# Optimization experiments

Hardware: AMD Instinct MI355X
Metric: run time of the kernel (lower is better)

Reference implementation:

```python
import jax, jax.numpy as jnp
import numpy as np

N_NODES = 100000
N_EDGES = 1600000
IN_CH = 64
OUT_CH = 64
NUM_K = 9  # (degree+1)^dim = 3*3 quadratic B-spline taps; equals prod(kernel_size) here


def _quad_basis(v):
    # torch_spline_conv quadratic basis for k_mod in {0,1,2}; v = frac(pseudo*(K-deg)) = pseudo here
    return jnp.stack([0.5 * v * v - v + 0.5,
                      -v * v + v + 0.5,
                      0.5 * v * v], axis=-1)  # [E,3]


def spline_conv(x, src, dst, pseudo, W, root, bias, n_nodes):
    # W: [9, C_in, C_out]; basis B: [E, 9]
    b0 = _quad_basis(pseudo[:, 0])          # [E,3]
    b1 = _quad_basis(pseudo[:, 1])          # [E,3]
    B = (b0[:, :, None] * b1[:, None, :]).reshape(pseudo.shape[0], NUM_K)  # [E,9]
    x_src = x[src]                           # gather [E, C_in]
    msg = B[:, 0:1] * (x_src @ W[0])
    for k in range(1, NUM_K):                # fixed small loop over kernel taps
        msg = msg + B[:, k:k + 1] * (x_src @ W[k])
    out = jax.ops.segment_sum(msg, dst, num_segments=n_nodes)  # scatter-add at targets
    return out + x @ root + bias


def setup_inputs() -> dict:
    key = jax.random.key(0)
    ks = jax.random.split(key, 10)
    x = jax.random.normal(ks[0], (N_NODES, IN_CH), dtype=jnp.float32)
    edge_index = jax.random.randint(ks[1], (2, N_EDGES), 0, N_NODES, dtype=jnp.int64)
    pseudo = jax.random.uniform(ks[2], (N_EDGES, 2), dtype=jnp.float32)
    s1 = 1.0 / np.sqrt(IN_CH * NUM_K)
    s2 = 1.0 / np.sqrt(OUT_CH * NUM_K)
    W1 = jax.random.normal(ks[3], (NUM_K, IN_CH, OUT_CH), dtype=jnp.float32) * s1
    root1 = jax.random.normal(ks[4], (IN_CH, OUT_CH), dtype=jnp.float32) * s1
    b1 = jax.random.normal(ks[5], (OUT_CH,), dtype=jnp.float32) * 0.01
    W2 = jax.random.normal(ks[6], (NUM_K, OUT_CH, OUT_CH), dtype=jnp.float32) * s2
    root2 = jax.random.normal(ks[7], (OUT_CH, OUT_CH), dtype=jnp.float32) * s2
    b2 = jax.random.normal(ks[8], (OUT_CH,), dtype=jnp.float32) * 0.01
    return {"x": x, "edge_index": edge_index, "pseudo": pseudo,
            "W1": W1, "root1": root1, "b1": b1,
            "W2": W2, "root2": root2, "b2": b2}


def reference(x, edge_index, pseudo, W1, root1, b1, W2, root2, b2):
    src, dst = edge_index[0], edge_index[1]  # PyG: aggregate messages at target
    h = jax.nn.relu(spline_conv(x, src, dst, pseudo, W1, root1, b1, N_NODES))
    h = jax.nn.relu(spline_conv(h, src, dst, pseudo, W2, root2, b2, N_NODES))
    return h
```

## Files before the change

### kernel.cpp

```cpp
#include <hip/hip_runtime.h>
#include <stdint.h>

typedef __attribute__((ext_vector_type(8))) short bf16x8;
typedef __attribute__((ext_vector_type(4))) float f32x4;

__device__ __forceinline__ float bf2f(unsigned short u) {
  union { unsigned int i; float f; } x; x.i = ((unsigned int)u) << 16; return x.f;
}
__device__ __forceinline__ unsigned short f2bf(float f) {
  union { float f; unsigned int i; } x; x.f = f;
  unsigned int i = x.i;
  return (unsigned short)((i + 0x7FFFu + ((i >> 16) & 1u)) >> 16);
}


__global__ void count_kernel(const int* __restrict__ ei, int E, int* __restrict__ counts) {
  int e = blockIdx.x * blockDim.x + threadIdx.x;
  if (e < E) atomicAdd(&counts[ei[E + e]], 1);
}

__global__ void scan1_kernel(const int* __restrict__ counts, int n, int* __restrict__ bsum) {
  int i = blockIdx.x * 256 + threadIdx.x;
  int v = (i < n) ? counts[i] : 0;
  int lane = threadIdx.x & 63, w = threadIdx.x >> 6;
  for (int d = 32; d > 0; d >>= 1) v += __shfl_down(v, d, 64);
  __shared__ int ws[4];
  if (lane == 0) ws[w] = v;
  __syncthreads();
  if (threadIdx.x == 0) bsum[blockIdx.x] = ws[0] + ws[1] + ws[2] + ws[3];
}

__global__ void scan2_kernel(int* __restrict__ bsum, int G) {
  int t = threadIdx.x;
  int c = (G + 511) >> 9;
  int lo = min(t * c, G), hi = min(lo + c, G);
  int s = 0;
  for (int i = lo; i < hi; ++i) s += bsum[i];
  int lane = t & 63, w = t >> 6;
  int incl = s;
  for (int d = 1; d < 64; d <<= 1) { int u = __shfl_up(incl, d, 64); if (lane >= d) incl += u; }
  __shared__ int wsum[8];
  if (lane == 63) wsum[w] = incl;
  __syncthreads();
  int wpre = 0;
  for (int i = 0; i < w; ++i) wpre += wsum[i];
  int excl = wpre + incl - s;
  for (int i = lo; i < hi; ++i) { int v = bsum[i]; bsum[i] = excl; excl += v; }
}

__global__ void scan3_kernel(const int* __restrict__ counts, int n, const int* __restrict__ bsum,
                             int* __restrict__ offsets, int* __restrict__ cursor, int total) {
  int i = blockIdx.x * 256 + threadIdx.x;
  int v = (i < n) ? counts[i] : 0;
  int lane = threadIdx.x & 63, w = threadIdx.x >> 6;
  int incl = v;
  for (int d = 1; d < 64; d <<= 1) { int u = __shfl_up(incl, d, 64); if (lane >= d) incl += u; }
  __shared__ int wsum[4];
  if (lane == 63) wsum[w] = incl;
  __syncthreads();
  int pre = bsum[blockIdx.x];
  for (int j = 0; j < w; ++j) pre += wsum[j];
  if (i < n) {
    int excl = pre + incl - v;
    offsets[i] = excl;
    cursor[i] = excl;
  }
  if (i == 0) offsets[n] = total;
}


__global__ void fill_kernel(const int* __restrict__ ei, const float* __restrict__ pseudo,
                            int E, int* __restrict__ cursor, int* __restrict__ src_s,
                            float2* __restrict__ bas) {
  int e = blockIdx.x * blockDim.x + threadIdx.x;
  if (e >= E) return;
  int d = ei[E + e];
  int s = ei[e];
  float2 uv = ((const float2*)pseudo)[e];
  float u = uv.x, v = uv.y;
  float b0 = 0.5f * u * u - u + 0.5f, b1 = -u * u + u + 0.5f, b2 = 0.5f * u * u;
  float c0 = 0.5f * v * v - v + 0.5f, c1 = -v * v + v + 0.5f, c2 = 0.5f * v * v;
  int p = atomicAdd(&cursor[d], 1);
  src_s[p] = s;
  size_t o = (size_t)p * 3;
  bas[o + 0] = make_float2(b0, b1);
  bas[o + 1] = make_float2(b2, c0);
  bas[o + 2] = make_float2(c1, c2);
}


__global__ void wconv_kernel(const float* __restrict__ W, const float* __restrict__ root,
                             unsigned short* __restrict__ Wt) {
  int i = blockIdx.x * blockDim.x + threadIdx.x;
  if (i >= 640 * 64) return;
  int co = i / 640, r = i % 640;
  float v = (r < 576) ? W[r * 64 + co] : root[(r - 576) * 64 + co];
  Wt[i] = f2bf(v);
}


__global__ void xconv_kernel(const float4* __restrict__ x4, ushort4* __restrict__ xh4, int n4) {
  int i = blockIdx.x * blockDim.x + threadIdx.x;
  if (i < n4) {
    float4 v = x4[i];
    ushort4 o;
    o.x = f2bf(v.x); o.y = f2bf(v.y); o.z = f2bf(v.z); o.w = f2bf(v.w);
    xh4[i] = o;
  }
}


#define SROW 648

#define EDGE_FMA(Q0, Q1, Q2, XV)                                   \
  {                                                                \
    float t0 = Q0.x * XV, t1 = Q0.y * XV, t2 = Q1.x * XV;          \
    a0 += t0 * Q1.y; a1 += t0 * Q2.x; a2 += t0 * Q2.y;             \
    a3 += t1 * Q1.y; a4 += t1 * Q2.x; a5 += t1 * Q2.y;             \
    a6 += t2 * Q1.y; a7 += t2 * Q2.x; a8 += t2 * Q2.y;             \
  }

template <bool OUTBF16>
__global__ __launch_bounds__(256) void fused_kernel(const int* __restrict__ offsets,
                                                    const int* __restrict__ src_s,
                                                    const float2* __restrict__ bas,
                                                    const unsigned short* __restrict__ Xh,
                                                    const unsigned short* __restrict__ Wt,
                                                    const float* __restrict__ bias,
                                                    void* __restrict__ outv, int N) {
  __shared__ short sA[16 * SROW];
  int tid = threadIdx.x, w = tid >> 6, lane = tid & 63;
  int nodeBase = blockIdx.x * 16;

  for (int t = 0; t < 4; ++t) {
    int row = w * 4 + t;
    int n = nodeBase + row;
    if (n >= N) continue;
    int beg = __builtin_amdgcn_readfirstlane(offsets[n]);
    int end = __builtin_amdgcn_readfirstlane(offsets[n + 1]);
    float a0 = 0.f, a1 = 0.f, a2 = 0.f, a3 = 0.f, a4 = 0.f,
          a5 = 0.f, a6 = 0.f, a7 = 0.f, a8 = 0.f;
    int j = beg;
    for (; j + 4 <= end; j += 4) {
      int s0 = src_s[j], s1 = src_s[j + 1], s2 = src_s[j + 2], s3 = src_s[j + 3];
      size_t o = (size_t)j * 3;
      float2 q00 = bas[o + 0], q01 = bas[o + 1], q02 = bas[o + 2];
      float2 q10 = bas[o + 3], q11 = bas[o + 4], q12 = bas[o + 5];
      float2 q20 = bas[o + 6], q21 = bas[o + 7], q22 = bas[o + 8];
      float2 q30 = bas[o + 9], q31 = bas[o + 10], q32 = bas[o + 11];
      float xv0 = bf2f(Xh[(size_t)s0 * 64 + lane]);
      float xv1 = bf2f(Xh[(size_t)s1 * 64 + lane]);
      float xv2 = bf2f(Xh[(size_t)s2 * 64 + lane]);
      float xv3 = bf2f(Xh[(size_t)s3 * 64 + lane]);
      EDGE_FMA(q00, q01, q02, xv0);
      EDGE_FMA(q10, q11, q12, xv1);
      EDGE_FMA(q20, q21, q22, xv2);
      EDGE_FMA(q30, q31, q32, xv3);
    }
    for (; j < end; ++j) {
      int s0 = src_s[j];
      size_t o = (size_t)j * 3;
      float2 q00 = bas[o + 0], q01 = bas[o + 1], q02 = bas[o + 2];
      float xv0 = bf2f(Xh[(size_t)s0 * 64 + lane]);
      EDGE_FMA(q00, q01, q02, xv0);
    }
    float self = bf2f(Xh[(size_t)n * 64 + lane]);
    int rb = row * SROW;
    sA[rb + 0 * 64 + lane] = (short)f2bf(a0);
    sA[rb + 1 * 64 + lane] = (short)f2bf(a1);
    sA[rb + 2 * 64 + lane] = (short)f2bf(a2);
    sA[rb + 3 * 64 + lane] = (short)f2bf(a3);
    sA[rb + 4 * 64 + lane] = (short)f2bf(a4);
    sA[rb + 5 * 64 + lane] = (short)f2bf(a5);
    sA[rb + 6 * 64 + lane] = (short)f2bf(a6);
    sA[rb + 7 * 64 + lane] = (short)f2bf(a7);
    sA[rb + 8 * 64 + lane] = (short)f2bf(a8);
    sA[rb + 576 + lane] = (short)f2bf(self);
  }
  __syncthreads();

  int r15 = lane & 15, kg = lane >> 4;
  f32x4 acc = {0.f, 0.f, 0.f, 0.f};
#pragma unroll
  for (int kk = 0; kk < 20; ++kk) {
    int kbase = kk * 32 + kg * 8;
    bf16x8 af = *(const bf16x8*)(&sA[r15 * SROW + kbase]);
    bf16x8 bfr = *(const bf16x8*)(Wt + (size_t)(w * 16 + r15) * 640 + kbase);
    acc = __builtin_amdgcn_mfma_f32_16x16x32_bf16(af, bfr, acc, 0, 0, 0);
  }
  int col = w * 16 + r15;
  float bv = bias[col];
  int row0 = kg * 4;
#pragma unroll
  for (int r = 0; r < 4; ++r) {
    int node = nodeBase + row0 + r;
    if (node < N) {
      float val = fmaxf(acc[r] + bv, 0.f);
      size_t idx = (size_t)node * 64 + col;
      if (OUTBF16) ((unsigned short*)outv)[idx] = f2bf(val);
      else ((float*)outv)[idx] = val;
    }
  }
}


extern "C" void kernel_launch(void* const* d_in, const int* in_sizes, int n_in,
                              void* d_out, int out_size, void* d_ws, size_t ws_size,
                              hipStream_t stream) {
  const float* x = (const float*)d_in[0];
  const int* ei = (const int*)d_in[1];
  const float* pseudo = (const float*)d_in[2];
  const float* W1 = (const float*)d_in[3];
  const float* root1 = (const float*)d_in[4];
  const float* b1 = (const float*)d_in[5];
  const float* W2 = (const float*)d_in[6];
  const float* root2 = (const float*)d_in[7];
  const float* b2 = (const float*)d_in[8];

  const int N = in_sizes[0] / 64;
  const int E = in_sizes[1] / 2;
  const int G = (N + 255) / 256;

  char* p = (char*)d_ws;
  auto carve = [&](size_t bytes) -> void* {
    void* r = (void*)p;
    p += (bytes + 255) & ~(size_t)255;
    return r;
  };
  int* counts = (int*)carve((size_t)N * 4);
  int* offsets = (int*)carve((size_t)(N + 1) * 4);
  int* cursor = (int*)carve((size_t)N * 4);
  int* bsum = (int*)carve((size_t)G * 4);
  int* src_s = (int*)carve((size_t)E * 4);
  float2* bas = (float2*)carve((size_t)E * 24);
  unsigned short* Wt1 = (unsigned short*)carve(640 * 64 * 2);
  unsigned short* Wt2 = (unsigned short*)carve(640 * 64 * 2);
  unsigned short* h = (unsigned short*)carve((size_t)N * 64 * 2);
  unsigned short* xh = (unsigned short*)carve((size_t)N * 64 * 2);
  (void)ws_size;

  hipMemsetAsync(counts, 0, (size_t)N * 4, stream);
  count_kernel<<<(E + 255) / 256, 256, 0, stream>>>(ei, E, counts);
  scan1_kernel<<<G, 256, 0, stream>>>(counts, N, bsum);
  scan2_kernel<<<1, 512, 0, stream>>>(bsum, G);
  scan3_kernel<<<G, 256, 0, stream>>>(counts, N, bsum, offsets, cursor, E);
  fill_kernel<<<(E + 255) / 256, 256, 0, stream>>>(ei, pseudo, E, cursor, src_s, bas);
  wconv_kernel<<<160, 256, 0, stream>>>(W1, root1, Wt1);
  wconv_kernel<<<160, 256, 0, stream>>>(W2, root2, Wt2);
  xconv_kernel<<<(N * 16 + 255) / 256, 256, 0, stream>>>((const float4*)x, (ushort4*)xh, N * 16);

  int FB = (N + 15) / 16;
  fused_kernel<true><<<FB, 256, 0, stream>>>(offsets, src_s, bas, xh, Wt1, b1, (void*)h, N);
  fused_kernel<false><<<FB, 256, 0, stream>>>(offsets, src_s, bas, h, Wt2, b2, d_out, N);
}
```

Measured before the change: 428.6 us.

## Pack edge records into 16-byte fp16 structs and double-buffer 8-edge loads

Replaces the separate src index array and 24-byte float basis array with one 16-byte record per edge: a pre-shifted byte offset plus six fp16 basis factors. Each record then comes from a single vector load. The gather loop now prefetches 8 records ahead with double buffering to overlap latency. Blocks grow to 512 threads, so each wave handles 2 nodes instead of 4, and only 4 of the 8 waves run the MFMA stage. The change cuts edge-stream bytes and raises memory parallelism, at the cost of fp16 precision on the basis values and idle waves during the matmul.

```diff
diff --git a/kernel.cpp b/kernel.cpp
--- a/kernel.cpp
+++ b/kernel.cpp
@@ -11,6 +11,19 @@
   union { float f; unsigned int i; } x; x.f = f;
   unsigned int i = x.i;
   return (unsigned short)((i + 0x7FFFu + ((i >> 16) & 1u)) >> 16);
+}
+__device__ __forceinline__ float f16lo(unsigned int u) {
+  union { unsigned short s; _Float16 h; } x; x.s = (unsigned short)(u & 0xFFFFu);
+  return (float)x.h;
+}
+__device__ __forceinline__ float f16hi(unsigned int u) {
+  union { unsigned short s; _Float16 h; } x; x.s = (unsigned short)(u >> 16);
+  return (float)x.h;
+}
+__device__ __forceinline__ unsigned int packf16(float a, float b) {
+  union { unsigned short s; _Float16 h; } x, y;
+  x.h = (_Float16)a; y.h = (_Float16)b;
+  return (unsigned int)x.s | ((unsigned int)y.s << 16);
 }
 
 
@@ -70,8 +83,7 @@
 
 
 __global__ void fill_kernel(const int* __restrict__ ei, const float* __restrict__ pseudo,
-                            int E, int* __restrict__ cursor, int* __restrict__ src_s,
-                            float2* __restrict__ bas) {
+                            int E, int* __restrict__ cursor, uint4* __restrict__ recs) {
   int e = blockIdx.x * blockDim.x + threadIdx.x;
   if (e >= E) return;
   int d = ei[E + e];
@@ -81,11 +93,12 @@
   float b0 = 0.5f * u * u - u + 0.5f, b1 = -u * u + u + 0.5f, b2 = 0.5f * u * u;
   float c0 = 0.5f * v * v - v + 0.5f, c1 = -v * v + v + 0.5f, c2 = 0.5f * v * v;
   int p = atomicAdd(&cursor[d], 1);
-  src_s[p] = s;
-  size_t o = (size_t)p * 3;
-  bas[o + 0] = make_float2(b0, b1);
-  bas[o + 1] = make_float2(b2, c0);
-  bas[o + 2] = make_float2(c1, c2);
+  uint4 r;
+  r.x = ((unsigned int)s) << 7;
+  r.y = packf16(b0, b1);
+  r.z = packf16(b2, c0);
+  r.w = packf16(c1, c2);
+  recs[p] = r;
 }
 
 
@@ -112,18 +125,27 @@
 
 #define SROW 648
 
-#define EDGE_FMA(Q0, Q1, Q2, XV)                                   \
-  {                                                                \
-    float t0 = Q0.x * XV, t1 = Q0.y * XV, t2 = Q1.x * XV;          \
-    a0 += t0 * Q1.y; a1 += t0 * Q2.x; a2 += t0 * Q2.y;             \
-    a3 += t1 * Q1.y; a4 += t1 * Q2.x; a5 += t1 * Q2.y;             \
-    a6 += t2 * Q1.y; a7 += t2 * Q2.x; a8 += t2 * Q2.y;             \
+#define LOAD8(R, jj)                                                     \
+  _Pragma("unroll") for (int k = 0; k < 8; ++k) R[k] = recs[(size_t)(jj) + k];
+
+#define PROC8(R)                                                         \
+  {                                                                      \
+    float xv[8];                                                         \
+    _Pragma("unroll") for (int k = 0; k < 8; ++k)                        \
+        xv[k] = bf2f(*(const unsigned short*)(Xb + R[k].x + laneB));     \
+    _Pragma("unroll") for (int k = 0; k < 8; ++k) {                      \
+      float b0 = f16lo(R[k].y), b1 = f16hi(R[k].y), b2 = f16lo(R[k].z);  \
+      float c0 = f16hi(R[k].z), c1 = f16lo(R[k].w), c2 = f16hi(R[k].w);  \
+      float t0 = b0 * xv[k], t1 = b1 * xv[k], t2 = b2 * xv[k];           \
+      a0 += t0 * c0; a1 += t0 * c1; a2 += t0 * c2;                       \
+      a3 += t1 * c0; a4 += t1 * c1; a5 += t1 * c2;                       \
+      a6 += t2 * c0; a7 += t2 * c1; a8 += t2 * c2;                       \
+    }                                                                    \
   }
 
 template <bool OUTBF16>
-__global__ __launch_bounds__(256) void fused_kernel(const int* __restrict__ offsets,
-                                                    const int* __restrict__ src_s,
-                                                    const float2* __restrict__ bas,
+__global__ __launch_bounds__(512) void fused_kernel(const int* __restrict__ offsets,
+                                                    const uint4* __restrict__ recs,
                                                     const unsigned short* __restrict__ Xh,
                                                     const unsigned short* __restrict__ Wt,
                                                     const float* __restrict__ bias,
@@ -131,74 +153,80 @@
   __shared__ short sA[16 * SROW];
   int tid = threadIdx.x, w = tid >> 6, lane = tid & 63;
   int nodeBase = blockIdx.x * 16;
-
-  for (int t = 0; t < 4; ++t) {
-    int row = w * 4 + t;
+  const char* Xb = (const char*)Xh;
+  unsigned int laneB = (unsigned int)lane * 2u;
+
+#pragma unroll
+  for (int t = 0; t < 2; ++t) {
+    int row = w * 2 + t;
     int n = nodeBase + row;
-    if (n >= N) continue;
-    int beg = __builtin_amdgcn_readfirstlane(offsets[n]);
-    int end = __builtin_amdgcn_readfirstlane(offsets[n + 1]);
-    float a0 = 0.f, a1 = 0.f, a2 = 0.f, a3 = 0.f, a4 = 0.f,
-          a5 = 0.f, a6 = 0.f, a7 = 0.f, a8 = 0.f;
-    int j = beg;
-    for (; j + 4 <= end; j += 4) {
-      int s0 = src_s[j], s1 = src_s[j + 1], s2 = src_s[j + 2], s3 = src_s[j + 3];
-      size_t o = (size_t)j * 3;
-      float2 q00 = bas[o + 0], q01 = bas[o + 1], q02 = bas[o + 2];
-      float2 q10 = bas[o + 3], q11 = bas[o + 4], q12 = bas[o + 5];
-      float2 q20 = bas[o + 6], q21 = bas[o + 7], q22 = bas[o + 8];
-      float2 q30 = bas[o + 9], q31 = bas[o + 10], q32 = bas[o + 11];
-      float xv0 = bf2f(Xh[(size_t)s0 * 64 + lane]);
-      float xv1 = bf2f(Xh[(size_t)s1 * 64 + lane]);
-      float xv2 = bf2f(Xh[(size_t)s2 * 64 + lane]);
-      float xv3 = bf2f(Xh[(size_t)s3 * 64 + lane]);
-      EDGE_FMA(q00, q01, q02, xv0);
-      EDGE_FMA(q10, q11, q12, xv1);
-      EDGE_FMA(q20, q21, q22, xv2);
-      EDGE_FMA(q30, q31, q32, xv3);
+    if (n < N) {
+      int beg = __builtin_amdgcn_readfirstlane(offsets[n]);
+      int end = __builtin_amdgcn_readfirstlane(offsets[n + 1]);
+      float a0 = 0.f, a1 = 0.f, a2 = 0.f, a3 = 0.f, a4 = 0.f,
+            a5 = 0.f, a6 = 0.f, a7 = 0.f, a8 = 0.f;
+      int j = beg;
+      int nfull = (end - beg) >> 3;
+      uint4 R0[8], R1[8];
+      if (nfull > 0) { LOAD8(R0, j); }
+      int b = 0;
+      while (b < nfull) {
+        if (b + 1 < nfull) { LOAD8(R1, j + 8); }
+        PROC8(R0);
+        j += 8; ++b;
+        if (b >= nfull) break;
+        if (b + 1 < nfull) { LOAD8(R0, j + 8); }
+        PROC8(R1);
+        j += 8; ++b;
+      }
+      for (; j < end; ++j) {
+        uint4 r = recs[j];
+        float xv = bf2f(*(const unsigned short*)(Xb + r.x + laneB));
+        float b0 = f16lo(r.y), b1 = f16hi(r.y), b2 = f16lo(r.z);
+        float c0 = f16hi(r.z), c1 = f16lo(r.w), c2 = f16hi(r.w);
+        float t0 = b0 * xv, t1 = b1 * xv, t2 = b2 * xv;
+        a0 += t0 * c0; a1 += t0 * c1; a2 += t0 * c2;
+        a3 += t1 * c0; a4 += t1 * c1; a5 += t1 * c2;
+        a6 += t2 * c0; a7 += t2 * c1; a8 += t2 * c2;
+      }
+      float self = bf2f(Xh[(size_t)n * 64 + lane]);
+      int rb = row * SROW;
+      sA[rb + 0 * 64 + lane] = (short)f2bf(a0);
+      sA[rb + 1 * 64 + lane] = (short)f2bf(a1);
+      sA[rb + 2 * 64 + lane] = (short)f2bf(a2);
+      sA[rb + 3 * 64 + lane] = (short)f2bf(a3);
+      sA[rb + 4 * 64 + lane] = (short)f2bf(a4);
+      sA[rb + 5 * 64 + lane] = (short)f2bf(a5);
+      sA[rb + 6 * 64 + lane] = (short)f2bf(a6);
+      sA[rb + 7 * 64 + lane] = (short)f2bf(a7);
+      sA[rb + 8 * 64 + lane] = (short)f2bf(a8);
+      sA[rb + 576 + lane] = (short)f2bf(self);
     }
-    for (; j < end; ++j) {
-      int s0 = src_s[j];
-      size_t o = (size_t)j * 3;
-      float2 q00 = bas[o + 0], q01 = bas[o + 1], q02 = bas[o + 2];
-      float xv0 = bf2f(Xh[(size_t)s0 * 64 + lane]);
-      EDGE_FMA(q00, q01, q02, xv0);
+  }
+  __syncthreads();
+
+  if (w < 4) {
+    int r15 = lane & 15, kg = lane >> 4;
+    f32x4 acc = {0.f, 0.f, 0.f, 0.f};
+#pragma unroll
+    for (int kk = 0; kk < 20; ++kk) {
+      int kbase = kk * 32 + kg * 8;
+      bf16x8 af = *(const bf16x8*)(&sA[r15 * SROW + kbase]);
+      bf16x8 bfr = *(const bf16x8*)(Wt + (size_t)(w * 16 + r15) * 640 + kbase);
+      acc = __builtin_amdgcn_mfma_f32_16x16x32_bf16(af, bfr, acc, 0, 0, 0);
     }
-    float self = bf2f(Xh[(size_t)n * 64 + lane]);
-    int rb = row * SROW;
-    sA[rb + 0 * 64 + lane] = (short)f2bf(a0);
-    sA[rb + 1 * 64 + lane] = (short)f2bf(a1);
-    sA[rb + 2 * 64 + lane] = (short)f2bf(a2);
-    sA[rb + 3 * 64 + lane] = (short)f2bf(a3);
-    sA[rb + 4 * 64 + lane] = (short)f2bf(a4);
-    sA[rb + 5 * 64 + lane] = (short)f2bf(a5);
-    sA[rb + 6 * 64 + lane] = (short)f2bf(a6);
-    sA[rb + 7 * 64 + lane] = (short)f2bf(a7);
-    sA[rb + 8 * 64 + lane] = (short)f2bf(a8);
-    sA[rb + 576 + lane] = (short)f2bf(self);
-  }
-  __syncthreads();
-
-  int r15 = lane & 15, kg = lane >> 4;
-  f32x4 acc = {0.f, 0.f, 0.f, 0.f};
+    int col = w * 16 + r15;
+    float bv = bias[col];
+    int row0 = kg * 4;
 #pragma unroll
-  for (int kk = 0; kk < 20; ++kk) {
-    int kbase = kk * 32 + kg * 8;
-    bf16x8 af = *(const bf16x8*)(&sA[r15 * SROW + kbase]);
-    bf16x8 bfr = *(const bf16x8*)(Wt + (size_t)(w * 16 + r15) * 640 + kbase);
-    acc = __builtin_amdgcn_mfma_f32_16x16x32_bf16(af, bfr, acc, 0, 0, 0);
-  }
-  int col = w * 16 + r15;
-  float bv = bias[col];
-  int row0 = kg * 4;
-#pragma unroll
-  for (int r = 0; r < 4; ++r) {
-    int node = nodeBase + row0 + r;
-    if (node < N) {
-      float val = fmaxf(acc[r] + bv, 0.f);
-      size_t idx = (size_t)node * 64 + col;
-      if (OUTBF16) ((unsigned short*)outv)[idx] = f2bf(val);
-      else ((float*)outv)[idx] = val;
+    for (int r = 0; r < 4; ++r) {
+      int node = nodeBase + row0 + r;
+      if (node < N) {
+        float val = fmaxf(acc[r] + bv, 0.f);
+        size_t idx = (size_t)node * 64 + col;
+        if (OUTBF16) ((unsigned short*)outv)[idx] = f2bf(val);
+        else ((float*)outv)[idx] = val;
+      }
     }
   }
 }
@@ -231,8 +259,7 @@
   int* offsets = (int*)carve((size_t)(N + 1) * 4);
   int* cursor = (int*)carve((size_t)N * 4);
   int* bsum = (int*)carve((size_t)G * 4);
-  int* src_s = (int*)carve((size_t)E * 4);
-  float2* bas = (float2*)carve((size_t)E * 24);
+  uint4* recs = (uint4*)carve((size_t)E * 16);
   unsigned short* Wt1 = (unsigned short*)carve(640 * 64 * 2);
   unsigned short* Wt2 = (unsigned short*)carve(640 * 64 * 2);
   unsigned short* h = (unsigned short*)carve((size_t)N * 64 * 2);
@@ -244,12 +271,12 @@
   scan1_kernel<<<G, 256, 0, stream>>>(counts, N, bsum);
   scan2_kernel<<<1, 512, 0, stream>>>(bsum, G);
   scan3_kernel<<<G, 256, 0, stream>>>(counts, N, bsum, offsets, cursor, E);
-  fill_kernel<<<(E + 255) / 256, 256, 0, stream>>>(ei, pseudo, E, cursor, src_s, bas);
+  fill_kernel<<<(E + 255) / 256, 256, 0, stream>>>(ei, pseudo, E, cursor, recs);
   wconv_kernel<<<160, 256, 0, stream>>>(W1, root1, Wt1);
   wconv_kernel<<<160, 256, 0, stream>>>(W2, root2, Wt2);
   xconv_kernel<<<(N * 16 + 255) / 256, 256, 0, stream>>>((const float4*)x, (ushort4*)xh, N * 16);
 
   int FB = (N + 15) / 16;
-  fused_kernel<true><<<FB, 256, 0, stream>>>(offsets, src_s, bas, xh, Wt1, b1, (void*)h, N);
-  fused_kernel<false><<<FB, 256, 0, stream>>>(offsets, src_s, bas, h, Wt2, b2, d_out, N);
-}
+  fused_kernel<true><<<FB, 512, 0, stream>>>(offsets, recs, xh, Wt1, b1, (void*)h, N);
+  fused_kernel<false><<<FB, 512, 0, stream>>>(offsets, recs, h, Wt2, b2, d_out, N);
+}
```

After: 469.5 us. +9.5%, slower.
